# Optimization experiments

Hardware: AMD Instinct MI355X
Metric: run time of the kernel (lower is better)

Reference implementation:

```python
import jax, jax.numpy as jnp
import numpy as np

N_NODES = 30000
N_EDGES = 300000
D_IN = 64
HID = 128
HEADS = 4
EDG = 2 * HID  # 256, num_edg_hiddens
OUT = 86
EPS = 1e-5
NEG_SLOPE = 0.2


def _kaiming(key, shape, fan_in):
    return jax.random.normal(key, shape, dtype=jnp.float32) * np.sqrt(2.0 / fan_in)


def _bn(x, w, b):
    # F.batch_norm(training=True): normalize with biased batch stats
    m = x.mean(axis=0)
    v = x.var(axis=0)
    return (x - m) / jnp.sqrt(v + EPS) * w + b


def _gat(x, src, dst, w, b, att_src, att_dst, n_nodes):
    # x: [N, Fin], w: [HEADS*HID, Fin] -> h: [N, HEADS, HID]
    h = (x @ w.T).reshape(x.shape[0], HEADS, -1)
    a_s = (h * att_src).sum(-1)  # [N, HEADS]
    a_d = (h * att_dst).sum(-1)  # [N, HEADS]
    alpha = jax.nn.leaky_relu(a_s[src] + a_d[dst], NEG_SLOPE)  # [E, HEADS]
    # segment softmax over destination node
    amax = jax.ops.segment_max(alpha, dst, num_segments=n_nodes)
    e = jnp.exp(alpha - amax[dst])
    denom = jax.ops.segment_sum(e, dst, num_segments=n_nodes)
    coef = e / denom[dst]  # [E, HEADS]
    out = jax.ops.segment_sum(h[src] * coef[:, :, None], dst, num_segments=n_nodes)
    return out.mean(axis=1) + b  # mean over heads (concat=False), [N, HID]


def setup_inputs() -> dict:
    key = jax.random.key(0)
    ks = jax.random.split(key, 16)
    x = jax.random.normal(ks[0], (N_NODES, D_IN), dtype=jnp.float32)
    edge_index = jax.random.randint(ks[1], (2, N_EDGES), 0, N_NODES, dtype=jnp.int32)
    return {
        'x': x,
        'edge_index': edge_index,
        'w0': _kaiming(ks[2], (HEADS * HID, D_IN), D_IN),
        'b0': jnp.zeros((HID,), jnp.float32),
        'ats0': _kaiming(ks[3], (1, HEADS, HID), HEADS * HID),
        'atd0': _kaiming(ks[4], (1, HEADS, HID), HEADS * HID),
        'bn1w': jnp.ones((HID,), jnp.float32),
        'bn1b': jnp.zeros((HID,), jnp.float32),
        'w2': _kaiming(ks[5], (HEADS * HID, HID), HID),
        'b2': jnp.zeros((HID,), jnp.float32),
        'ats1': _kaiming(ks[6], (1, HEADS, HID), HEADS * HID),
        'atd1': _kaiming(ks[7], (1, HEADS, HID), HEADS * HID),
        'bn2w': jnp.ones((HID,), jnp.float32),
        'bn2b': jnp.zeros((HID,), jnp.float32),
        'w4': _kaiming(ks[8], (EDG, EDG), EDG),
        'b4': jnp.zeros((EDG,), jnp.float32),
        'bn3w': jnp.ones((EDG,), jnp.float32),
        'bn3b': jnp.zeros((EDG,), jnp.float32),
        'w6': _kaiming(ks[9], (EDG, EDG), EDG),
        'b6': jnp.zeros((EDG,), jnp.float32),
        'bn4w': jnp.ones((EDG,), jnp.float32),
        'bn4b': jnp.zeros((EDG,), jnp.float32),
        'w8': _kaiming(ks[10], (OUT, EDG), EDG),
        'b8': jnp.zeros((OUT,), jnp.float32),
    }


def reference(x, edge_index, w0, b0, ats0, atd0, bn1w, bn1b, w2, b2, ats1, atd1,
              bn2w, bn2b, w4, b4, bn3w, bn3b, w6, b6, bn4w, bn4b, w8, b8):
    src, dst = edge_index[0], edge_index[1]
    n = x.shape[0]
    h = _gat(x, src, dst, w0, b0, ats0, atd0, n)
    x1 = jax.nn.relu(_bn(h, bn1w, bn1b))
    h = _gat(x1, src, dst, w2, b2, ats1, atd1, n)
    xr = jax.nn.relu(_bn(h, bn2w, bn2b) + x1)
    # edge feature MLP with residuals
    ef1 = jnp.concatenate([xr[src], xr[dst]], axis=1)  # [E, 2*HID]
    ef = _bn(ef1 @ w4.T + b4, bn3w, bn3b)
    ef1 = jax.nn.relu(ef + ef1)
    ef = _bn(ef1 @ w6.T + b6, bn4w, bn4b)
    ef = jax.nn.relu(ef + ef1)
    return ef @ w8.T + b8  # [E, OUT]
```

## Files before the change

kernel.cpp:

```cpp
#include <hip/hip_runtime.h>
#include <hip/hip_bf16.h>
#include <stdint.h>

typedef __hip_bfloat16 bf16;
typedef unsigned int u32;
typedef __attribute__((ext_vector_type(8))) short short8;
typedef __attribute__((ext_vector_type(4))) float f32x4;
typedef __attribute__((ext_vector_type(2))) float f32x2;

#define NNODES 30000
#define NEDGES 300000
#define NODE_PAD 30080
#define EDGE_PAD 300032
#define NCH128 2344
#define NEG_SLOPE 0.2f
#define BN_EPS 1e-5f

__device__ __forceinline__ float b2f(short s) {
  u32 u = ((u32)(unsigned short)s) << 16;
  return __uint_as_float(u);
}
__device__ __forceinline__ short f2b(float f) {
  bf16 h = __float2bfloat16(f);
  return *(short*)&h;
}

__device__ __forceinline__ void gload16(const void* g, void* l) {
  __builtin_amdgcn_global_load_lds(
      (__attribute__((address_space(1))) unsigned int*)(uintptr_t)g,
      (__attribute__((address_space(3))) unsigned int*)(uintptr_t)l, 16, 0, 0);
}


__global__ void zfill(u32* __restrict__ p, int n) {
  int i = blockIdx.x * 256 + threadIdx.x;
  if (i < n) p[i] = 0u;
}

__global__ void fillpat(u32* __restrict__ p, u32 v, int n) {
  int i = blockIdx.x * 256 + threadIdx.x;
  if (i < n) p[i] = v;
}

__global__ void cvt_bf16_pad(const float* __restrict__ src, bf16* __restrict__ dst,
                             int rows_valid, int total, int cols) {
  int i = blockIdx.x * 256 + threadIdx.x;
  if (i >= total) return;
  int r = i / cols;
  float v = (r < rows_valid) ? src[i] : 0.f;
  dst[i] = __float2bfloat16(v);
}

__global__ void cvt_w45(const float* __restrict__ w4, bf16* __restrict__ w45b) {
  int i = blockIdx.x * 256 + threadIdx.x;
  if (i >= 512 * 128) return;
  int n = i >> 7, k = i & 127;
  float v = (n < 256) ? w4[n * 256 + k] : w4[(n - 256) * 256 + 128 + k];
  w45b[i] = __float2bfloat16(v);
}

__global__ void bn_coef(const float* __restrict__ stats, const float* __restrict__ w,
                        const float* __restrict__ b, int n, float invN,
                        float* __restrict__ sc, float* __restrict__ sh) {
  int c = threadIdx.x;
  if (c >= n) return;
  float m = stats[c] * invN;
  float var = stats[n + c] * invN - m * m;
  float rstd = rsqrtf(var + BN_EPS);
  sc[c] = rstd * w[c];
  sh[c] = b[c] - m * rstd * w[c];
}

__global__ __launch_bounds__(256) void gemm_bt(
    const bf16* __restrict__ A, const bf16* __restrict__ B, bf16* __restrict__ Cout,
    int K, int ldc, int Mvalid, int Nvalid) {
  __shared__ __align__(16) short smA[2][128 * 64];
  __shared__ __align__(16) short smB[2][128 * 64];
  const int tid = threadIdx.x;
  const int lane = tid & 63;
  const int wid = tid >> 6;
  const int wr = wid >> 1, wc = wid & 1;
  const size_t arow0 = (size_t)blockIdx.x * 128;
  const size_t brow0 = (size_t)blockIdx.y * 128;
  f32x4 acc[4][4] = {};
  const int nk = K >> 6;

  int srow[4], scol[4];
#pragma unroll
  for (int i = 0; i < 4; ++i) {
    int s = i * 256 + tid;
    srow[i] = s >> 3;
    scol[i] = ((s & 7) ^ ((s >> 3) & 7)) * 8;
  }
  auto stage = [&](int buf, int kt) {
#pragma unroll
    for (int i = 0; i < 4; ++i) {
      int s = i * 256 + tid;
      gload16(A + (arow0 + srow[i]) * K + kt * 64 + scol[i], &smA[buf][s * 8]);
      gload16(B + (brow0 + srow[i]) * K + kt * 64 + scol[i], &smB[buf][s * 8]);
    }
  };
  auto compute = [&](int buf) {
#pragma unroll
    for (int ks = 0; ks < 2; ++ks) {
      short8 af[4], bfr[4];
      const int cg = ks * 4 + (lane >> 4);
#pragma unroll
      for (int m = 0; m < 4; ++m) {
        int row = wr * 64 + m * 16 + (lane & 15);
        af[m] = *(const short8*)&smA[buf][row * 64 + ((cg ^ (row & 7)) << 3)];
      }
#pragma unroll
      for (int n = 0; n < 4; ++n) {
        int row = wc * 64 + n * 16 + (lane & 15);
        bfr[n] = *(const short8*)&smB[buf][row * 64 + ((cg ^ (row & 7)) << 3)];
      }
#pragma unroll
      for (int m = 0; m < 4; ++m)
#pragma unroll
        for (int n = 0; n < 4; ++n)
          acc[m][n] = __builtin_amdgcn_mfma_f32_16x16x32_bf16(af[m], bfr[n], acc[m][n], 0, 0, 0);
    }
  };

  stage(0, 0);
  __syncthreads();
  int cur = 0;
  for (int kt = 0; kt < nk; ++kt) {
    if (kt + 1 < nk) stage(cur ^ 1, kt + 1);
    compute(cur);
    __syncthreads();
    cur ^= 1;
  }

  const int rbase = (int)arow0 + wr * 64 + (lane >> 4) * 4;
  const int cbase = (int)brow0 + wc * 64 + (lane & 15);
#pragma unroll
  for (int m = 0; m < 4; ++m) {
#pragma unroll
    for (int n = 0; n < 4; ++n) {
      int col = cbase + n * 16;
      if (col >= Nvalid) continue;
#pragma unroll
      for (int r = 0; r < 4; ++r) {
        int row = rbase + m * 16 + r;
        if (row < Mvalid)
          Cout[(size_t)row * ldc + col] = __float2bfloat16(acc[m][n][r]);
      }
    }
  }
}

__global__ __launch_bounds__(512, 2) void gemm2_v8(
    const bf16* __restrict__ A, const bf16* __restrict__ Bw, bf16* __restrict__ C,
    float* __restrict__ statsOut) {
  __shared__ __align__(16) short smA[2][128 * 256];
  const int tid = threadIdx.x;
  const int lane = tid & 63;
  const int wid = tid >> 6;
  const int lr = lane & 15, lk = lane >> 4;

  short8 bfrag[2][8];
#pragma unroll
  for (int n = 0; n < 2; ++n)
#pragma unroll
    for (int ks = 0; ks < 8; ++ks)
      bfrag[n][ks] = *(const short8*)(Bw + (size_t)(wid * 32 + n * 16 + lr) * 256 + (ks * 4 + lk) * 8);

  auto stage = [&](int buf, int chunk) {
    const bf16* Ab = A + (size_t)chunk * 128 * 256;
#pragma unroll
    for (int i = 0; i < 8; ++i) {
      int s = i * 512 + tid;
      int p = s >> 10;
      int row = (s >> 3) & 127;
      int c8 = s & 7;
      gload16(Ab + row * 256 + (p * 8 + (c8 ^ (row & 7))) * 8, &smA[buf][s * 8]);
    }
  };

  float ss[2] = {}, sq[2] = {};

  auto compute = [&](int buf, int chunk) {
    f32x4 acc[8][2];
#pragma unroll
    for (int g = 0; g < 8; ++g) { acc[g][0] = {}; acc[g][1] = {}; }
#pragma unroll
    for (int ks = 0; ks < 8; ++ks) {
      const int p = ks >> 1;
      const int cgl = (ks & 1) * 4 + lk;
#pragma unroll
      for (int g = 0; g < 8; ++g) {
        int row = g * 16 + lr;
        short8 af = *(const short8*)&smA[buf][p * 8192 + row * 64 + ((cgl ^ (row & 7)) << 3)];
        acc[g][0] = __builtin_amdgcn_mfma_f32_16x16x32_bf16(af, bfrag[0][ks], acc[g][0], 0, 0, 0);
        acc[g][1] = __builtin_amdgcn_mfma_f32_16x16x32_bf16(af, bfrag[1][ks], acc[g][1], 0, 0, 0);
      }
    }
    size_t rbase = (size_t)chunk * 128;
#pragma unroll
    for (int g = 0; g < 8; ++g) {
#pragma unroll
      for (int n = 0; n < 2; ++n) {
        int col = wid * 32 + n * 16 + lr;
#pragma unroll
        for (int j = 0; j < 4; ++j) {
          float v = acc[g][n][j];
          ss[n] += v;
          sq[n] += v * v;
          C[(rbase + g * 16 + lk * 4 + j) * 256 + col] = __float2bfloat16(v);
        }
      }
    }
  };

  int c = blockIdx.x;
  stage(0, c);
  __syncthreads();
  int buf = 0;
  while (true) {
    int nx = c + (int)gridDim.x;
    if (nx < NCH128) stage(buf ^ 1, nx);
    compute(buf, c);
    if (nx >= NCH128) break;
    __syncthreads();
    buf ^= 1;
    c = nx;
  }

#pragma unroll
  for (int n = 0; n < 2; ++n) {
    float s = ss[n], q = sq[n];
    s += __shfl_xor(s, 16); s += __shfl_xor(s, 32);
    q += __shfl_xor(q, 16); q += __shfl_xor(q, 32);
    if (lk == 0) {
      atomicAdd(&statsOut[wid * 32 + n * 16 + lr], s);
      atomicAdd(&statsOut[256 + wid * 32 + n * 16 + lr], q);
    }
  }
}

__global__ __launch_bounds__(256, 2) void gemm3_v3(
    const bf16* __restrict__ Y, const bf16* __restrict__ E, const bf16* __restrict__ Bw,
    float* __restrict__ Cout, const float* __restrict__ scf, const float* __restrict__ shf,
    const float* __restrict__ bias) {
  __shared__ __align__(16) short smW[96 * 256];
  __shared__ __align__(16) short smA[64 * 256];
  const int tid = threadIdx.x;
  const int lane = tid & 63;
  const int wid = tid >> 6;
  const int lr = lane & 15, lk = lane >> 4;

#pragma unroll
  for (int i = 0; i < 12; ++i) {
    int s = i * 256 + tid;
    int row = s >> 5, c8 = s & 31;
    gload16(Bw + row * 256 + (c8 ^ (row & 7)) * 8, &smW[s * 8]);
  }

  const int cb = (tid & 31) * 8;
  f32x4 sc0 = *(const f32x4*)&scf[cb];
  f32x4 sc1 = *(const f32x4*)&scf[cb + 4];
  f32x4 sh0 = *(const f32x4*)&shf[cb];
  f32x4 sh1 = *(const f32x4*)&shf[cb + 4];
  float bb[6][4];
#pragma unroll
  for (int f = 0; f < 6; ++f)
#pragma unroll
    for (int r = 0; r < 4; ++r) {
      int n = f * 16 + lk * 4 + r;
      bb[f][r] = (n < 86) ? bias[n] : 0.f;
    }

  short8 y[8], e[8];
  auto loadYE = [&](int t) {
    size_t base = (size_t)t * 64 * 256;
#pragma unroll
    for (int j = 0; j < 8; ++j) {
      size_t off = base + (size_t)(j * 256 + tid) * 8;
      y[j] = *(const short8*)(Y + off);
      e[j] = *(const short8*)(E + off);
    }
  };

  const int NT = EDGE_PAD / 64;
  int t = blockIdx.x;
  loadYE(t);
  __syncthreads();

  while (true) {
#pragma unroll
    for (int j = 0; j < 8; ++j) {
      int s = j * 256 + tid;
      int row = s >> 5, c8 = s & 31;
      short8 o;
#pragma unroll
      for (int jj = 0; jj < 4; ++jj) {
        o[jj]     = f2b(fmaxf(b2f(y[j][jj]) * sc0[jj] + sh0[jj] + b2f(e[j][jj]), 0.f));
        o[jj + 4] = f2b(fmaxf(b2f(y[j][jj + 4]) * sc1[jj] + sh1[jj] + b2f(e[j][jj + 4]), 0.f));
      }
      *(short8*)&smA[row * 256 + ((c8 ^ (row & 7)) << 3)] = o;
    }
    __syncthreads();
    int cur = t;
    int nx = t + (int)gridDim.x;
    if (nx < NT) loadYE(nx);

    f32x4 acc[6] = {};
#pragma unroll
    for (int ks = 0; ks < 8; ++ks) {
      int cg = ks * 4 + lk;
      int ra = wid * 16 + lr;
      short8 af = *(const short8*)&smA[ra * 256 + ((cg ^ (ra & 7)) << 3)];
#pragma unroll
      for (int f = 0; f < 6; ++f) {
        int rw = f * 16 + lr;
        short8 wf = *(const short8*)&smW[rw * 256 + ((cg ^ (rw & 7)) << 3)];
        acc[f] = __builtin_amdgcn_mfma_f32_16x16x32_bf16(wf, af, acc[f], 0, 0, 0);
      }
    }

    int rbase = cur * 64 + wid * 16;
    if (rbase < NEDGES) {
      float* gp = Cout + (size_t)(rbase + lr) * 86;
#pragma unroll
      for (int f = 0; f < 6; ++f) {
        int n0 = f * 16 + lk * 4;
        if (n0 + 1 < 86) {
          f32x2 v;
          v[0] = acc[f][0] + bb[f][0];
          v[1] = acc[f][1] + bb[f][1];
          *(f32x2*)(gp + n0) = v;
        }
        if (n0 + 3 < 86) {
          f32x2 v;
          v[0] = acc[f][2] + bb[f][2];
          v[1] = acc[f][3] + bb[f][3];
          *(f32x2*)(gp + n0 + 2) = v;
        }
      }
    }
    if (nx >= NT) break;
    t = nx;
    __syncthreads();
  }
}


__global__ __launch_bounds__(256) void att_reduce(
    const bf16* __restrict__ h, const float* __restrict__ ats, const float* __restrict__ atd,
    float* __restrict__ a_s, float* __restrict__ a_d) {
  int n = blockIdx.x;
  int lane = threadIdx.x & 63;
  int hd = threadIdx.x >> 6;
  const bf16* hp = h + (size_t)n * 512 + hd * 128;
  const float* sw = ats + hd * 128;
  const float* dw = atd + hd * 128;
  float h1 = __bfloat162float(hp[lane]), h2 = __bfloat162float(hp[lane + 64]);
  float s = h1 * sw[lane] + h2 * sw[lane + 64];
  float d = h1 * dw[lane] + h2 * dw[lane + 64];
#pragma unroll
  for (int off = 32; off > 0; off >>= 1) {
    s += __shfl_down(s, off);
    d += __shfl_down(d, off);
  }
  if (lane == 0) {
    a_s[n * 4 + hd] = s;
    a_d[n * 4 + hd] = d;
  }
}

__global__ void edge_alpha_max(const int* __restrict__ ei, const float* __restrict__ a_s,
                               const float* __restrict__ a_d, float* __restrict__ alphaE,
                               u32* __restrict__ amaxU) {
  int t = blockIdx.x * 256 + threadIdx.x;
  if (t >= NEDGES * 4) return;
  int e = t >> 2, h = t & 3;
  int s = ei[e], d = ei[NEDGES + e];
  float a = a_s[s * 4 + h] + a_d[d * 4 + h];
  a = (a > 0.f) ? a : NEG_SLOPE * a;
  alphaE[t] = a;
  u32 bits = __float_as_uint(a);
  u32 key = bits ^ (((int)bits < 0) ? 0xFFFFFFFFu : 0x80000000u);
  atomicMax(&amaxU[d * 4 + h], key);
}

__global__ void edge_exp_sum(const int* __restrict__ ei, float* __restrict__ alphaE,
                             const u32* __restrict__ amaxU, float* __restrict__ denom) {
  int t = blockIdx.x * 256 + threadIdx.x;
  if (t >= NEDGES * 4) return;
  int e = t >> 2, h = t & 3;
  int d = ei[NEDGES + e];
  u32 k = amaxU[d * 4 + h];
  u32 bits = (k & 0x80000000u) ? (k ^ 0x80000000u) : ~k;
  float am = __uint_as_float(bits);
  float ev = __expf(alphaE[t] - am);
  alphaE[t] = ev;
  atomicAdd(&denom[d * 4 + h], ev);
}

__global__ void edge_scatter(const int* __restrict__ ei, const bf16* __restrict__ hbuf,
                             const float* __restrict__ evals, const float* __restrict__ denom,
                             float* __restrict__ agg) {
  int e = blockIdx.x * 2 + (threadIdx.x >> 7);
  int d = threadIdx.x & 127;
  int s = ei[e], dd = ei[NEDGES + e];
  const short* hp = (const short*)hbuf + (size_t)s * 512 + d;
  float sum = 0.f;
#pragma unroll
  for (int h = 0; h < 4; ++h) {
    float coef = evals[e * 4 + h] / denom[dd * 4 + h];
    sum += b2f(hp[h * 128]) * coef;
  }
  atomicAdd(&agg[dd * 128 + d], sum * 0.25f);
}


__global__ __launch_bounds__(256) void col_stats128(const float* __restrict__ X,
                                                    float* __restrict__ stats, int rows) {
  __shared__ float smS[8][128], smQ[8][128];
  int t = threadIdx.x;
  int sub = t >> 5;
  int c4 = (t & 31) * 4;
  int rend = blockIdx.x * 64 + 64;
  if (rend > rows) rend = rows;
  f32x4 s = {}, q = {};
  for (int r = blockIdx.x * 64 + sub; r < rend; r += 8) {
    f32x4 v = *(const f32x4*)&X[(size_t)r * 128 + c4];
    s += v;
    q += v * v;
  }
  *(f32x4*)&smS[sub][c4] = s;
  *(f32x4*)&smQ[sub][c4] = q;
  __syncthreads();
  if (t < 128) {
    float ts = 0.f, tq = 0.f;
#pragma unroll
    for (int g = 0; g < 8; ++g) { ts += smS[g][t]; tq += smQ[g][t]; }
    atomicAdd(&stats[t], ts);
    atomicAdd(&stats[128 + t], tq);
  }
}

__global__ void bn_relu_node(const float* __restrict__ agg, const float* __restrict__ stats,
                             const float* __restrict__ w, const float* __restrict__ b,
                             bf16* __restrict__ xout) {
  int i = blockIdx.x * 256 + threadIdx.x;
  if (i >= NODE_PAD * 128) return;
  int r = i >> 7, c = i & 127;
  float v = 0.f;
  if (r < NNODES) {
    float m = stats[c] * (1.f / NNODES);
    float var = stats[128 + c] * (1.f / NNODES) - m * m;
    float rstd = rsqrtf(var + BN_EPS);
    v = fmaxf((agg[i] - m) * rstd * w[c] + b[c], 0.f);
  }
  xout[i] = __float2bfloat16(v);
}

__global__ void bn_res_relu_node(const float* __restrict__ agg, const float* __restrict__ stats,
                                 const float* __restrict__ w, const float* __restrict__ b,
                                 const bf16* __restrict__ x1b, bf16* __restrict__ xrb) {
  int i = blockIdx.x * 256 + threadIdx.x;
  if (i >= NODE_PAD * 128) return;
  int r = i >> 7, c = i & 127;
  float v = 0.f;
  if (r < NNODES) {
    float m = stats[c] * (1.f / NNODES);
    float var = stats[128 + c] * (1.f / NNODES) - m * m;
    float rstd = rsqrtf(var + BN_EPS);
    v = fmaxf((agg[i] - m) * rstd * w[c] + b[c] + __bfloat162float(x1b[i]), 0.f);
  }
  xrb[i] = __float2bfloat16(v);
}

__device__ __forceinline__ void accum_edge(short8 pa, short8 qa, bf16* __restrict__ y1out,
                                           size_t obase, f32x4& s0, f32x4& s1,
                                           f32x4& q0, f32x4& q1) {
  short8 o;
  float v[8];
#pragma unroll
  for (int j = 0; j < 8; ++j) {
    v[j] = b2f(pa[j]) + b2f(qa[j]);
    o[j] = f2b(v[j]);
  }
  *(short8*)(y1out + obase) = o;
  s0[0] += v[0]; s0[1] += v[1]; s0[2] += v[2]; s0[3] += v[3];
  s1[0] += v[4]; s1[1] += v[5]; s1[2] += v[6]; s1[3] += v[7];
  q0[0] += v[0] * v[0]; q0[1] += v[1] * v[1]; q0[2] += v[2] * v[2]; q0[3] += v[3] * v[3];
  q1[0] += v[4] * v[4]; q1[1] += v[5] * v[5]; q1[2] += v[6] * v[6]; q1[3] += v[7] * v[7];
}

__global__ __launch_bounds__(256) void e_stats_mat(const int* __restrict__ ei,
                                                   const bf16* __restrict__ PQ,
                                                   bf16* __restrict__ y1out,
                                                   float* __restrict__ stats) {
  __shared__ float smS[8][256], smQ[8][256];
  int t = threadIdx.x;
  int sub = t >> 5;
  int c8 = (t & 31) * 8;
  int ebase = blockIdx.x * 128 + sub * 16;
  f32x4 s0 = {}, s1 = {}, q0 = {}, q1 = {};
#pragma unroll 1
  for (int i = 0; i < 16; i += 4) {
    int e = ebase + i;
    if (e + 3 < NEDGES) {
      int4 sn = *(const int4*)&ei[e];
      int4 dn = *(const int4*)&ei[NEDGES + e];
      short8 p0 = *(const short8*)&PQ[(size_t)sn.x * 512 + c8];
      short8 p1 = *(const short8*)&PQ[(size_t)sn.y * 512 + c8];
      short8 p2 = *(const short8*)&PQ[(size_t)sn.z * 512 + c8];
      short8 p3 = *(const short8*)&PQ[(size_t)sn.w * 512 + c8];
      short8 r0 = *(const short8*)&PQ[(size_t)dn.x * 512 + 256 + c8];
      short8 r1 = *(const short8*)&PQ[(size_t)dn.y * 512 + 256 + c8];
      short8 r2 = *(const short8*)&PQ[(size_t)dn.z * 512 + 256 + c8];
      short8 r3 = *(const short8*)&PQ[(size_t)dn.w * 512 + 256 + c8];
      accum_edge(p0, r0, y1out, (size_t)e * 256 + c8, s0, s1, q0, q1);
      accum_edge(p1, r1, y1out, (size_t)(e + 1) * 256 + c8, s0, s1, q0, q1);
      accum_edge(p2, r2, y1out, (size_t)(e + 2) * 256 + c8, s0, s1, q0, q1);
      accum_edge(p3, r3, y1out, (size_t)(e + 3) * 256 + c8, s0, s1, q0, q1);
    } else {
      for (int j = 0; j < 4; ++j) {
        int ej = e + j;
        if (ej >= NEDGES) break;
        int sn = ei[ej], dn = ei[NEDGES + ej];
        short8 p = *(const short8*)&PQ[(size_t)sn * 512 + c8];
        short8 r = *(const short8*)&PQ[(size_t)dn * 512 + 256 + c8];
        accum_edge(p, r, y1out, (size_t)ej * 256 + c8, s0, s1, q0, q1);
      }
    }
  }
  *(f32x4*)&smS[sub][c8] = s0;
  *(f32x4*)&smS[sub][c8 + 4] = s1;
  *(f32x4*)&smQ[sub][c8] = q0;
  *(f32x4*)&smQ[sub][c8 + 4] = q1;
  __syncthreads();
  float ts = 0.f, tq = 0.f;
#pragma unroll
  for (int g = 0; g < 8; ++g) { ts += smS[g][t]; tq += smQ[g][t]; }
  atomicAdd(&stats[t], ts);
  atomicAdd(&stats[256 + t], tq);
}

__global__ __launch_bounds__(256) void ef2_norm(const int* __restrict__ ei,
                                                const bf16* __restrict__ xrb,
                                                const float* __restrict__ stats,
                                                const float* __restrict__ w,
                                                const float* __restrict__ b,
                                                bf16* __restrict__ ef2) {
  int t = threadIdx.x;
  int e = blockIdx.x * 8 + (t >> 5);
  int c8 = (t & 31) * 8;
  size_t base = (size_t)e * 256 + c8;
  short8 out = {};
  if (e < NEDGES) {
    int node = (c8 < 128) ? ei[e] : ei[NEDGES + e];
    short8 yv = *(const short8*)&ef2[base];
    short8 res = *(const short8*)&xrb[(size_t)node * 128 + (c8 & 127)];
#pragma unroll
    for (int j = 0; j < 8; ++j) {
      int c = c8 + j;
      float m = stats[c] * (1.f / NEDGES);
      float var = stats[256 + c] * (1.f / NEDGES) - m * m;
      float rstd = rsqrtf(var + BN_EPS);
      float v = (b2f(yv[j]) - m) * rstd * w[c] + b[c] + b2f(res[j]);
      out[j] = f2b(fmaxf(v, 0.f));
    }
  }
  *(short8*)&ef2[base] = out;
}


extern "C" void kernel_launch(void* const* d_in, const int* in_sizes, int n_in,
                              void* d_out, int out_size, void* d_ws, size_t ws_size,
                              hipStream_t stream) {
  const float* x    = (const float*)d_in[0];
  const int*   ei   = (const int*)d_in[1];
  const float* w0   = (const float*)d_in[2];
  const float* ats0 = (const float*)d_in[4];
  const float* atd0 = (const float*)d_in[5];
  const float* bn1w = (const float*)d_in[6];
  const float* bn1b = (const float*)d_in[7];
  const float* w2   = (const float*)d_in[8];
  const float* ats1 = (const float*)d_in[10];
  const float* atd1 = (const float*)d_in[11];
  const float* bn2w = (const float*)d_in[12];
  const float* bn2b = (const float*)d_in[13];
  const float* w4   = (const float*)d_in[14];
  const float* bn3w = (const float*)d_in[16];
  const float* bn3b = (const float*)d_in[17];
  const float* w6   = (const float*)d_in[18];
  const float* bn4w = (const float*)d_in[20];
  const float* bn4b = (const float*)d_in[21];
  const float* w8   = (const float*)d_in[22];
  const float* b8   = (const float*)d_in[23];

  const size_t REG = 153616384;
  char* ws = (char*)d_ws;
  bf16*  ef2b = (bf16*)ws;
  char*  R    = ws + REG;
  bf16*  hb    = (bf16*)(R);
  bf16*  xb    = (bf16*)(R + 61603840);
  bf16*  x1b   = (bf16*)(R + 65454080);
  bf16*  xrb   = (bf16*)(R + 73154560);
  float* a_s   = (float*)(R + 80855040);
  float* a_d   = (float*)(R + 81335040);
  u32*   amaxU = (u32*)  (R + 81815040);
  float* denom = (float*)(R + 82295040);
  float* alphaE= (float*)(R + 82775040);
  float* agg   = (float*)(R + 87575040);
  bf16*  PQ    = hb;
  bf16*  y2b   = (bf16*)R;
  char*  S     = ws + 2 * REG;
  bf16*  w0b   = (bf16*)(S);
  bf16*  w2b   = (bf16*)(S + 65536);
  bf16*  w45b  = (bf16*)(S + 196608);
  bf16*  w6b   = (bf16*)(S + 327680);
  bf16*  w8pb  = (bf16*)(S + 458752);
  float* stats1= (float*)(S + 524288);
  float* stats2= (float*)(S + 526336);
  float* sc2   = (float*)(S + 528384);
  float* sh2   = (float*)(S + 529408);
  const size_t needed = 2 * REG + 530432;
  if (ws_size < needed) {
    fillpat<<<(out_size + 255) / 256, 256, 0, stream>>>((u32*)d_out, 0x7F7F7F7Fu, out_size);
    return;
  }

  cvt_bf16_pad<<<(NODE_PAD * 64 + 255) / 256, 256, 0, stream>>>(x, xb, NNODES, NODE_PAD * 64, 64);
  cvt_bf16_pad<<<(512 * 64 + 255) / 256, 256, 0, stream>>>(w0, w0b, 512, 512 * 64, 64);
  cvt_bf16_pad<<<(512 * 128 + 255) / 256, 256, 0, stream>>>(w2, w2b, 512, 512 * 128, 128);
  cvt_w45<<<(512 * 128 + 255) / 256, 256, 0, stream>>>(w4, w45b);
  cvt_bf16_pad<<<(256 * 256 + 255) / 256, 256, 0, stream>>>(w6, w6b, 256, 256 * 256, 256);
  cvt_bf16_pad<<<(128 * 256 + 255) / 256, 256, 0, stream>>>(w8, w8pb, 86, 128 * 256, 256);

  const int etb = (NEDGES * 4 + 255) / 256;

  gemm_bt<<<dim3(NODE_PAD / 128, 4), 256, 0, stream>>>(xb, w0b, hb, 64, 512, NODE_PAD, 512);
  att_reduce<<<NNODES, 256, 0, stream>>>(hb, ats0, atd0, a_s, a_d);
  zfill<<<(240000 + 255) / 256, 256, 0, stream>>>(amaxU, 240000);
  zfill<<<(3840000 + 255) / 256, 256, 0, stream>>>((u32*)agg, 3840000);
  edge_alpha_max<<<etb, 256, 0, stream>>>(ei, a_s, a_d, alphaE, amaxU);
  edge_exp_sum<<<etb, 256, 0, stream>>>(ei, alphaE, amaxU, denom);
  edge_scatter<<<NEDGES / 2, 256, 0, stream>>>(ei, hb, alphaE, denom, agg);
  zfill<<<1, 256, 0, stream>>>((u32*)stats1, 256);
  col_stats128<<<(NNODES + 63) / 64, 256, 0, stream>>>(agg, stats1, NNODES);
  bn_relu_node<<<NODE_PAD * 128 / 256, 256, 0, stream>>>(agg, stats1, bn1w, bn1b, x1b);

  gemm_bt<<<dim3(NODE_PAD / 128, 4), 256, 0, stream>>>(x1b, w2b, hb, 128, 512, NODE_PAD, 512);
  att_reduce<<<NNODES, 256, 0, stream>>>(hb, ats1, atd1, a_s, a_d);
  zfill<<<(240000 + 255) / 256, 256, 0, stream>>>(amaxU, 240000);
  zfill<<<(3840000 + 255) / 256, 256, 0, stream>>>((u32*)agg, 3840000);
  edge_alpha_max<<<etb, 256, 0, stream>>>(ei, a_s, a_d, alphaE, amaxU);
  edge_exp_sum<<<etb, 256, 0, stream>>>(ei, alphaE, amaxU, denom);
  edge_scatter<<<NEDGES / 2, 256, 0, stream>>>(ei, hb, alphaE, denom, agg);
  zfill<<<1, 256, 0, stream>>>((u32*)stats1, 256);
  col_stats128<<<(NNODES + 63) / 64, 256, 0, stream>>>(agg, stats1, NNODES);
  bn_res_relu_node<<<NODE_PAD * 128 / 256, 256, 0, stream>>>(agg, stats1, bn2w, bn2b, x1b, xrb);

  gemm_bt<<<dim3(NODE_PAD / 128, 4), 256, 0, stream>>>(xrb, w45b, PQ, 128, 512, NODE_PAD, 512);
  zfill<<<2, 256, 0, stream>>>((u32*)stats1, 512);
  e_stats_mat<<<(NEDGES + 127) / 128, 256, 0, stream>>>(ei, PQ, ef2b, stats1);
  ef2_norm<<<EDGE_PAD / 8, 256, 0, stream>>>(ei, xrb, stats1, bn3w, bn3b, ef2b);
  zfill<<<2, 256, 0, stream>>>((u32*)stats2, 512);
  gemm2_v8<<<586, 512, 0, stream>>>(ef2b, w6b, y2b, stats2);
  bn_coef<<<1, 256, 0, stream>>>(stats2, bn4w, bn4b, 256, 1.f / NEDGES, sc2, sh2);
  gemm3_v3<<<2344, 256, 0, stream>>>(y2b, ef2b, w8pb, (float*)d_out, sc2, sh2, b8);
}
```

Before: 814.5 us.

## Replace atomic edge-wise GAT softmax/scatter with CSR per-node gather aggregation

```diff
diff --git a/kernel.cpp b/kernel.cpp
--- a/kernel.cpp
+++ b/kernel.cpp
@@ -15,6 +15,7 @@
 #define NCH128 2344
 #define NEG_SLOPE 0.2f
 #define BN_EPS 1e-5f
+#define MAXD 128
 
 __device__ __forceinline__ float b2f(short s) {
   u32 u = ((u32)(unsigned short)s) << 16;
@@ -69,6 +70,96 @@
   float rstd = rsqrtf(var + BN_EPS);
   sc[c] = rstd * w[c];
   sh[c] = b[c] - m * rstd * w[c];
+}
+
+
+__global__ void csr_hist(const int* __restrict__ ei, u32* __restrict__ cnt) {
+  int e = blockIdx.x * 256 + threadIdx.x;
+  if (e >= NEDGES) return;
+  atomicAdd(&cnt[ei[NEDGES + e]], 1u);
+}
+
+__global__ __launch_bounds__(256) void scan30k(const u32* __restrict__ cnt,
+                                               u32* __restrict__ rowptr) {
+  __shared__ u32 part[256];
+  int t = threadIdx.x;
+  const int CH = (NNODES + 255) / 256;
+  int i0 = t * CH;
+  int i1 = i0 + CH;
+  if (i1 > NNODES) i1 = NNODES;
+  u32 s = 0;
+  for (int i = i0; i < i1; ++i) s += cnt[i];
+  part[t] = s;
+  __syncthreads();
+  for (int off = 1; off < 256; off <<= 1) {
+    u32 v = (t >= off) ? part[t - off] : 0u;
+    __syncthreads();
+    part[t] += v;
+    __syncthreads();
+  }
+  u32 run = (t == 0) ? 0u : part[t - 1];
+  for (int i = i0; i < i1; ++i) {
+    rowptr[i] = run;
+    run += cnt[i];
+  }
+  if (t == 255) rowptr[NNODES] = run;
+}
+
+__global__ void csr_fill(const int* __restrict__ ei, const u32* __restrict__ rowptr,
+                         u32* __restrict__ fill, u32* __restrict__ csrc) {
+  int e = blockIdx.x * 256 + threadIdx.x;
+  if (e >= NEDGES) return;
+  int dst = ei[NEDGES + e];
+  u32 pos = rowptr[dst] + atomicAdd(&fill[dst], 1u);
+  csrc[pos] = (u32)ei[e];
+}
+
+__global__ __launch_bounds__(256) void gat_agg(
+    const u32* __restrict__ rowptr, const u32* __restrict__ csrc,
+    const float* __restrict__ a_s, const float* __restrict__ a_d,
+    const bf16* __restrict__ hb, float* __restrict__ agg) {
+  __shared__ float al[2][MAXD][4];
+  __shared__ u32 srcl[2][MAXD];
+  const int sub = threadIdx.x >> 7;
+  const int d = threadIdx.x & 127;
+  const int node = blockIdx.x * 2 + sub;
+  u32 r0 = rowptr[node], r1 = rowptr[node + 1];
+  int deg = (int)(r1 - r0);
+  if (deg > MAXD) deg = MAXD;
+  if (d < deg) {
+    u32 s = csrc[r0 + d];
+    srcl[sub][d] = s;
+#pragma unroll
+    for (int hh = 0; hh < 4; ++hh) {
+      float a = a_s[s * 4 + hh] + a_d[node * 4 + hh];
+      al[sub][d][hh] = (a > 0.f) ? a : NEG_SLOPE * a;
+    }
+  }
+  __syncthreads();
+  if (d < 4 && deg > 0) {
+    float mx = -1e30f;
+    for (int e = 0; e < deg; ++e) mx = fmaxf(mx, al[sub][e][d]);
+    float sum = 0.f;
+    for (int e = 0; e < deg; ++e) {
+      float v = __expf(al[sub][e][d] - mx);
+      al[sub][e][d] = v;
+      sum += v;
+    }
+    float inv = 1.f / sum;
+    for (int e = 0; e < deg; ++e) al[sub][e][d] *= inv;
+  }
+  __syncthreads();
+  float acc = 0.f;
+  const short* hp = (const short*)hb;
+#pragma unroll 1
+  for (int e = 0; e < deg; ++e) {
+    u32 s = srcl[sub][e];
+    const short* row = hp + (size_t)s * 512 + d;
+    f32x4 c = *(const f32x4*)&al[sub][e][0];
+    acc += c[0] * b2f(row[0]) + c[1] * b2f(row[128]) +
+           c[2] * b2f(row[256]) + c[3] * b2f(row[384]);
+  }
+  agg[(size_t)node * 128 + d] = acc * 0.25f;
 }
 
 __global__ __launch_bounds__(256) void gemm_bt(
@@ -368,51 +459,6 @@
     a_s[n * 4 + hd] = s;
     a_d[n * 4 + hd] = d;
   }
-}
-
-__global__ void edge_alpha_max(const int* __restrict__ ei, const float* __restrict__ a_s,
-                               const float* __restrict__ a_d, float* __restrict__ alphaE,
-                               u32* __restrict__ amaxU) {
-  int t = blockIdx.x * 256 + threadIdx.x;
-  if (t >= NEDGES * 4) return;
-  int e = t >> 2, h = t & 3;
-  int s = ei[e], d = ei[NEDGES + e];
-  float a = a_s[s * 4 + h] + a_d[d * 4 + h];
-  a = (a > 0.f) ? a : NEG_SLOPE * a;
-  alphaE[t] = a;
-  u32 bits = __float_as_uint(a);
-  u32 key = bits ^ (((int)bits < 0) ? 0xFFFFFFFFu : 0x80000000u);
-  atomicMax(&amaxU[d * 4 + h], key);
-}
-
-__global__ void edge_exp_sum(const int* __restrict__ ei, float* __restrict__ alphaE,
-                             const u32* __restrict__ amaxU, float* __restrict__ denom) {
-  int t = blockIdx.x * 256 + threadIdx.x;
-  if (t >= NEDGES * 4) return;
-  int e = t >> 2, h = t & 3;
-  int d = ei[NEDGES + e];
-  u32 k = amaxU[d * 4 + h];
-  u32 bits = (k & 0x80000000u) ? (k ^ 0x80000000u) : ~k;
-  float am = __uint_as_float(bits);
-  float ev = __expf(alphaE[t] - am);
-  alphaE[t] = ev;
-  atomicAdd(&denom[d * 4 + h], ev);
-}
-
-__global__ void edge_scatter(const int* __restrict__ ei, const bf16* __restrict__ hbuf,
-                             const float* __restrict__ evals, const float* __restrict__ denom,
-                             float* __restrict__ agg) {
-  int e = blockIdx.x * 2 + (threadIdx.x >> 7);
-  int d = threadIdx.x & 127;
-  int s = ei[e], dd = ei[NEDGES + e];
-  const short* hp = (const short*)hbuf + (size_t)s * 512 + d;
-  float sum = 0.f;
-#pragma unroll
-  for (int h = 0; h < 4; ++h) {
-    float coef = evals[e * 4 + h] / denom[dd * 4 + h];
-    sum += b2f(hp[h * 128]) * coef;
-  }
-  atomicAdd(&agg[dd * 128 + d], sum * 0.25f);
 }
 
 
@@ -605,9 +651,9 @@
   bf16*  xrb   = (bf16*)(R + 73154560);
   float* a_s   = (float*)(R + 80855040);
   float* a_d   = (float*)(R + 81335040);
-  u32*   amaxU = (u32*)  (R + 81815040);
-  float* denom = (float*)(R + 82295040);
-  float* alphaE= (float*)(R + 82775040);
+  u32*   rowptr= (u32*)  (R + 81815040);
+  u32*   cntf  = (u32*)  (R + 82295040);
+  u32*   csrc  = (u32*)  (R + 82775040);
   float* agg   = (float*)(R + 87575040);
   bf16*  PQ    = hb;
   bf16*  y2b   = (bf16*)R;
@@ -634,26 +680,24 @@
   cvt_bf16_pad<<<(256 * 256 + 255) / 256, 256, 0, stream>>>(w6, w6b, 256, 256 * 256, 256);
   cvt_bf16_pad<<<(128 * 256 + 255) / 256, 256, 0, stream>>>(w8, w8pb, 86, 128 * 256, 256);
 
-  const int etb = (NEDGES * 4 + 255) / 256;
+  const int eb = (NEDGES + 255) / 256;
+
+  zfill<<<(NNODES + 255) / 256, 256, 0, stream>>>(cntf, NNODES);
+  csr_hist<<<eb, 256, 0, stream>>>(ei, cntf);
+  scan30k<<<1, 256, 0, stream>>>(cntf, rowptr);
+  zfill<<<(NNODES + 255) / 256, 256, 0, stream>>>(cntf, NNODES);
+  csr_fill<<<eb, 256, 0, stream>>>(ei, rowptr, cntf, csrc);
 
   gemm_bt<<<dim3(NODE_PAD / 128, 4), 256, 0, stream>>>(xb, w0b, hb, 64, 512, NODE_PAD, 512);
   att_reduce<<<NNODES, 256, 0, stream>>>(hb, ats0, atd0, a_s, a_d);
-  zfill<<<(240000 + 255) / 256, 256, 0, stream>>>(amaxU, 240000);
-  zfill<<<(3840000 + 255) / 256, 256, 0, stream>>>((u32*)agg, 3840000);
-  edge_alpha_max<<<etb, 256, 0, stream>>>(ei, a_s, a_d, alphaE, amaxU);
-  edge_exp_sum<<<etb, 256, 0, stream>>>(ei, alphaE, amaxU, denom);
-  edge_scatter<<<NEDGES / 2, 256, 0, stream>>>(ei, hb, alphaE, denom, agg);
+  gat_agg<<<NNODES / 2, 256, 0, stream>>>(rowptr, csrc, a_s, a_d, hb, agg);
   zfill<<<1, 256, 0, stream>>>((u32*)stats1, 256);
   col_stats128<<<(NNODES + 63) / 64, 256, 0, stream>>>(agg, stats1, NNODES);
   bn_relu_node<<<NODE_PAD * 128 / 256, 256, 0, stream>>>(agg, stats1, bn1w, bn1b, x1b);
 
   gemm_bt<<<dim3(NODE_PAD / 128, 4), 256, 0, stream>>>(x1b, w2b, hb, 128, 512, NODE_PAD, 512);
   att_reduce<<<NNODES, 256, 0, stream>>>(hb, ats1, atd1, a_s, a_d);
-  zfill<<<(240000 + 255) / 256, 256, 0, stream>>>(amaxU, 240000);
-  zfill<<<(3840000 + 255) / 256, 256, 0, stream>>>((u32*)agg, 3840000);
-  edge_alpha_max<<<etb, 256, 0, stream>>>(ei, a_s, a_d, alphaE, amaxU);
-  edge_exp_sum<<<etb, 256, 0, stream>>>(ei, alphaE, amaxU, denom);
-  edge_scatter<<<NEDGES / 2, 256, 0, stream>>>(ei, hb, alphaE, denom, agg);
+  gat_agg<<<NNODES / 2, 256, 0, stream>>>(rowptr, csrc, a_s, a_d, hb, agg);
   zfill<<<1, 256, 0, stream>>>((u32*)stats1, 256);
   col_stats128<<<(NNODES + 63) / 64, 256, 0, stream>>>(agg, stats1, NNODES);
   bn_res_relu_node<<<NODE_PAD * 128 / 256, 256, 0, stream>>>(agg, stats1, bn2w, bn2b, x1b, xrb);
```

After: 682.8 us. -16.2%, faster.
